# Kernel tuning notes

Measured on AMD Instinct MI355X. Metric: run time of the kernel, lower is better.

The kernel has to match this reference:

```python
import jax, jax.numpy as jnp
import numpy as np

# Static config (matches init_kwargs)
N = 1024        # node_num
F = 64          # input_dim (window length)
D = 64          # dim == embed_dim (heads=1)
TOPK = 20
B = 64
EPS = 1e-5      # BatchNorm eps
NEG_SLOPE = 0.2 # GraphLayer leaky_relu slope


def setup_inputs() -> dict:
    key = jax.random.key(0)
    ks = jax.random.split(key, 12)
    s = lambda fan: 1.0 / np.sqrt(fan)
    inp = {
        'data': jax.random.normal(ks[0], (B, N, F), jnp.float32),
        'org_edge_index': jax.random.randint(ks[1], (2, 2048), 0, N),
        'embedding': jax.random.normal(ks[2], (N, D), jnp.float32) * s(D),   # nn.Embedding(node_num, dim), xavier-ish
        'lin_w': jax.random.normal(ks[3], (F, D), jnp.float32) * s(F),       # GraphLayer lin (bias=False)
        'att_i': jax.random.normal(ks[4], (D,), jnp.float32) * s(D),
        'att_j': jax.random.normal(ks[5], (D,), jnp.float32) * s(D),
        'att_em_i': jax.random.normal(ks[6], (D,), jnp.float32) * s(D),
        'att_em_j': jax.random.normal(ks[7], (D,), jnp.float32) * s(D),
        'gnn_bias': jnp.zeros((D,), jnp.float32),
        'bn1_gamma': jnp.ones((D,), jnp.float32),  # GNNLayer.bn
        'bn1_beta': jnp.zeros((D,), jnp.float32),
        'bn2_gamma': jnp.ones((D,), jnp.float32),  # bn_outlayer_in
        'bn2_beta': jnp.zeros((D,), jnp.float32),
        'out_w': jax.random.normal(ks[8], (D, 1), jnp.float32) * s(D),       # OutLayer Linear(dim, 1)
        'out_b': jnp.zeros((1,), jnp.float32),
    }
    return inp


def _batchnorm(x, gamma, beta, axes):
    # training-mode BatchNorm: batch statistics over `axes`, per-feature affine
    mu = jnp.mean(x, axis=axes, keepdims=True)
    var = jnp.var(x, axis=axes, keepdims=True)
    return gamma * (x - mu) * jax.lax.rsqrt(var + EPS) + beta


def reference(data, org_edge_index, embedding, lin_w, att_i, att_j, att_em_i,
              att_em_j, gnn_bias, bn1_gamma, bn1_beta, bn2_gamma, bn2_beta,
              out_w, out_b):
    # --- dynamic graph construction from embedding cosine similarity ---
    w = jax.lax.stop_gradient(embedding)          # weights_arr.detach()
    nrm = jnp.linalg.norm(w, axis=-1)
    cos = (w @ w.T) / jnp.clip(nrm[:, None] * nrm[None, :], 1e-10)
    _, topi = jax.lax.top_k(cos, TOPK)            # [N, TOPK] neighbors j of each target i
    # (torch code drops edges whose cos value is exactly 0 -- measure-zero with
    #  random embeddings; edge count stays N*TOPK. Self edge i->i is always in topk,
    #  matching remove_self_loops + add_self_loops.)

    # --- GraphLayer (GAT-style, heads=1, concat=False, aggr='add') ---
    xl = jnp.einsum('bnf,fd->bnd', data, lin_w)   # linear transform, [B,N,D]
    xj = xl[:, topi]                               # gather neighbor feats [B,N,TOPK,D]
    ej = embedding[topi]                           # neighbor embeddings [N,TOPK,D]
    # alpha = <key_i, att_i||att_em_i> + <key_j, att_j||att_em_j>
    score = (xl @ att_i)[:, :, None] \
          + (embedding @ att_em_i)[None, :, None] \
          + jnp.einsum('bnkd,d->bnk', xj, att_j) \
          + (ej @ att_em_j)[None]                  # [B,N,TOPK]
    alpha = jax.nn.softmax(jax.nn.leaky_relu(score, NEG_SLOPE), axis=-1)
    gnn = jnp.einsum('bnk,bnkd->bnd', alpha, xj) + gnn_bias

    # GNNLayer.bn: BatchNorm1d over B*N samples, D channels
    gnn = _batchnorm(gnn, bn1_gamma, bn1_beta, axes=(0, 1))

    # --- readout ---
    out = gnn * embedding[None]                    # mul with node embedding
    out = jax.nn.relu(_batchnorm(out, bn2_gamma, bn2_beta, axes=(0, 1)))
    # dropout(0.2) -> identity (eval)
    pred = (out @ out_w + out_b).reshape(B, N)     # OutLayer: Linear(D, 1)
    return pred, out
```

## Files before the change

kernel.cpp:

```cpp
#include <hip/hip_runtime.h>

#define NN 1024
#define KK 20
#define BN 65536
#define NEG_SLOPE 0.2f

typedef unsigned short u16;
typedef unsigned int u32;
typedef unsigned long long u64;
typedef __attribute__((ext_vector_type(8))) short bf8;
typedef __attribute__((ext_vector_type(4))) float f32x4;

__device__ __forceinline__ float bf2f(u16 h) {
    return __uint_as_float(((u32)h) << 16);
}
__device__ __forceinline__ u16 f2bf(float f) {
    u32 u = __float_as_uint(f);
    u32 lsb = (u >> 16) & 1u;
    u += 0x7fffu + lsb;
    return (u16)(u >> 16);
}
__device__ __forceinline__ void up2(u32 w, float& a, float& b) {
    a = __uint_as_float(w << 16);
    b = __uint_as_float(w & 0xffff0000u);
}
__device__ __forceinline__ bool is_bf(const void* g1) {
    return *(const u32*)g1 == 0x3F803F80u;
}
template <bool BF>
__device__ __forceinline__ float ldf(const void* p, size_t i) {
    if (BF) return bf2f(((const u16*)p)[i]);
    return ((const float*)p)[i];
}
template <bool BF>
__device__ __forceinline__ void stf(void* p, size_t i, float v) {
    if (BF) ((u16*)p)[i] = f2bf(v);
    else ((float*)p)[i] = v;
}
template <bool BF>
__device__ __forceinline__ void ldf2(const void* p, size_t pairidx, float& a, float& b) {
    if (BF) {
        u32 w = ((const u32*)p)[pairidx];
        up2(w, a, b);
    } else {
        float2 v = ((const float2*)p)[pairidx];
        a = v.x;
        b = v.y;
    }
}

template <bool BF>
__device__ void k1a_body(const void* emb, const void* aei, const void* aej,
                         u16* nwH, u16* nwL, float* e_i, float* e_j, float* stats) {
    __shared__ float sme[4][64], sm2[4][64];
    int tid = threadIdx.x;
    int lane = tid & 63, wave = tid >> 6;
    int n = blockIdx.x * 4 + wave;
    float v = ldf<BF>(emb, n * 64 + lane);
    sme[wave][lane] = v;
    sm2[wave][lane] = v * v;
    float s2 = v * v;
    float si = v * ldf<BF>(aei, lane);
    float sj = v * ldf<BF>(aej, lane);
#pragma unroll
    for (int off = 32; off; off >>= 1) {
        s2 += __shfl_xor(s2, off, 64);
        si += __shfl_xor(si, off, 64);
        sj += __shfl_xor(sj, off, 64);
    }
    float rq = rsqrtf(fmaxf(s2, 1e-20f));
    float x = v * rq;
    u16 h = f2bf(x);
    nwH[n * 64 + lane] = h;
    nwL[n * 64 + lane] = f2bf(x - bf2f(h));
    if (lane == 0) { e_i[n] = si; e_j[n] = sj; }
    __syncthreads();
    if (tid < 64) {
        float u1 = sme[0][tid] + sme[1][tid] + sme[2][tid] + sme[3][tid];
        atomicAdd(&stats[320 + tid], 64.f * u1);
    } else if (tid < 128) {
        int d = tid - 64;
        float u2 = sm2[0][d] + sm2[1][d] + sm2[2][d] + sm2[3][d];
        atomicAdd(&stats[384 + d], 64.f * u2);
    }
}
__global__ __launch_bounds__(256) void k1a_norm(const void* emb, const void* aei, const void* aej,
                                                const void* probe, u16* nwH, u16* nwL,
                                                float* e_i, float* e_j, float* stats) {
    if (is_bf(probe)) k1a_body<true>(emb, aei, aej, nwH, nwL, e_i, e_j, stats);
    else k1a_body<false>(emb, aei, aej, nwH, nwL, e_i, e_j, stats);
}

__global__ __launch_bounds__(256) void k1b_gram(const u16* __restrict__ nwH,
                                                const u16* __restrict__ nwL,
                                                float* __restrict__ G) {
    int tid = threadIdx.x;
    int lane = tid & 63, wave = tid >> 6;
    int c = lane & 15, quad = lane >> 4;
    int rowblk = blockIdx.x >> 4, colblk = blockIdx.x & 15;
    int arow = rowblk * 64 + wave * 16 + c;
    bf8 aH[2], aL[2];
#pragma unroll
    for (int s = 0; s < 2; ++s) {
        aH[s] = *(const bf8*)(nwH + (size_t)arow * 64 + s * 32 + quad * 8);
        aL[s] = *(const bf8*)(nwL + (size_t)arow * 64 + s * 32 + quad * 8);
    }
    f32x4 acc[4] = {{0.f, 0.f, 0.f, 0.f}, {0.f, 0.f, 0.f, 0.f}, {0.f, 0.f, 0.f, 0.f}, {0.f, 0.f, 0.f, 0.f}};
#pragma unroll
    for (int t = 0; t < 4; ++t) {
        int bnode = colblk * 64 + t * 16 + c;
#pragma unroll
        for (int s = 0; s < 2; ++s) {
            bf8 bH = *(const bf8*)(nwH + (size_t)bnode * 64 + s * 32 + quad * 8);
            bf8 bL = *(const bf8*)(nwL + (size_t)bnode * 64 + s * 32 + quad * 8);
            acc[t] = __builtin_amdgcn_mfma_f32_16x16x32_bf16(aH[s], bH, acc[t], 0, 0, 0);
            acc[t] = __builtin_amdgcn_mfma_f32_16x16x32_bf16(aH[s], bL, acc[t], 0, 0, 0);
            acc[t] = __builtin_amdgcn_mfma_f32_16x16x32_bf16(aL[s], bH, acc[t], 0, 0, 0);
        }
    }
#pragma unroll
    for (int t = 0; t < 4; ++t) {
#pragma unroll
        for (int reg = 0; reg < 4; ++reg) {
            int row = rowblk * 64 + wave * 16 + quad * 4 + reg;
            G[(size_t)row * 1024 + colblk * 64 + t * 16 + c] = acc[t][reg];
        }
    }
}

__device__ void k1c_body(int blk, const float* __restrict__ G, int* __restrict__ topi) {
    int lane = threadIdx.x & 63, wave = threadIdx.x >> 6;
    int n = blk * 4 + wave;
    const f32x4* gp = (const f32x4*)(G + (size_t)n * 1024 + lane * 16);
    f32x4 v0 = gp[0], v1 = gp[1], v2 = gp[2], v3 = gp[3];
    float c[16] = {v0.x, v0.y, v0.z, v0.w, v1.x, v1.y, v1.z, v1.w,
                   v2.x, v2.y, v2.z, v2.w, v3.x, v3.y, v3.z, v3.w};
    u32 o[16];
#pragma unroll
    for (int j = 0; j < 16; ++j) {
        u32 u = __float_as_uint(c[j]);
        o[j] = u ^ (u32)(((int)u >> 31) | 0x80000000);
    }
    unsigned mask = 0u;
    int keep = 0;
    for (int r = 0; r < KK; ++r) {
        u32 bo = 0u;
        int bj = 0;
#pragma unroll
        for (int j = 0; j < 16; ++j) {
            bool t = !((mask >> j) & 1u) && o[j] > bo;
            bo = t ? o[j] : bo;
            bj = t ? j : bj;
        }
        u64 key = ((u64)bo << 32) | (u32)(~(u32)(lane * 16 + bj));
#pragma unroll
        for (int off = 32; off; off >>= 1) {
            u64 ok = __shfl_xor((unsigned long long)key, off, 64);
            key = ok > key ? ok : key;
        }
        int bm = (int)((~(u32)key) & 1023u);
        if ((bm >> 4) == lane) mask |= 1u << (bm & 15);
        if (lane == r) keep = bm;
    }
    if (lane < KK) topi[n * KK + lane] = keep;
}

template <bool BF>
__device__ void k2_body(int blk, const void* data, const void* lin_w, const void* att_i,
                        const void* att_j, u16* xl, float* a_i, float* a_j) {
    __shared__ u16 Bl[64 * 72];
    __shared__ u16 Ct[64 * 72];
    int tid = threadIdx.x;
    {
        int k = tid >> 2, n0 = (tid & 3) * 16;
        if (BF) {
            const u16* lw = (const u16*)lin_w;
#pragma unroll
            for (int i = 0; i < 16; ++i) Bl[(n0 + i) * 72 + k] = lw[k * 64 + n0 + i];
        } else {
            const float* lw = (const float*)lin_w;
#pragma unroll
            for (int i = 0; i < 16; ++i) Bl[(n0 + i) * 72 + k] = f2bf(lw[k * 64 + n0 + i]);
        }
    }
    __syncthreads();
    int lane = tid & 63, wave = tid >> 6;
    int c = lane & 15, quad = lane >> 4;
    int m0 = blk * 64 + wave * 16;
    size_t row = (size_t)(m0 + c);
    f32x4 acc[4] = {{0.f, 0.f, 0.f, 0.f}, {0.f, 0.f, 0.f, 0.f}, {0.f, 0.f, 0.f, 0.f}, {0.f, 0.f, 0.f, 0.f}};
#pragma unroll
    for (int s = 0; s < 2; ++s) {
        bf8 a;
        if (BF) {
            a = *(const bf8*)((const u16*)data + row * 64 + s * 32 + quad * 8);
        } else {
            const float* dp = (const float*)data + row * 64 + s * 32 + quad * 8;
            f32x4 x0 = *(const f32x4*)dp;
            f32x4 x1 = *(const f32x4*)(dp + 4);
            a[0] = (short)f2bf(x0.x); a[1] = (short)f2bf(x0.y);
            a[2] = (short)f2bf(x0.z); a[3] = (short)f2bf(x0.w);
            a[4] = (short)f2bf(x1.x); a[5] = (short)f2bf(x1.y);
            a[6] = (short)f2bf(x1.z); a[7] = (short)f2bf(x1.w);
        }
#pragma unroll
        for (int t = 0; t < 4; ++t) {
            bf8 b = *(const bf8*)&Bl[(t * 16 + c) * 72 + s * 32 + quad * 8];
            acc[t] = __builtin_amdgcn_mfma_f32_16x16x32_bf16(a, b, acc[t], 0, 0, 0);
        }
    }
    float wi[4], wj[4];
#pragma unroll
    for (int t = 0; t < 4; ++t) {
        wi[t] = ldf<BF>(att_i, t * 16 + c);
        wj[t] = ldf<BF>(att_j, t * 16 + c);
    }
    float ai4[4] = {0.f, 0.f, 0.f, 0.f}, aj4[4] = {0.f, 0.f, 0.f, 0.f};
#pragma unroll
    for (int t = 0; t < 4; ++t) {
#pragma unroll
        for (int reg = 0; reg < 4; ++reg) {
            float v = acc[t][reg];
            Ct[(wave * 16 + quad * 4 + reg) * 72 + t * 16 + c] = f2bf(v);
            ai4[reg] += v * wi[t];
            aj4[reg] += v * wj[t];
        }
    }
#pragma unroll
    for (int reg = 0; reg < 4; ++reg) {
#pragma unroll
        for (int off = 1; off < 16; off <<= 1) {
            ai4[reg] += __shfl_xor(ai4[reg], off, 64);
            aj4[reg] += __shfl_xor(aj4[reg], off, 64);
        }
    }
    if (c == 0) {
#pragma unroll
        for (int reg = 0; reg < 4; ++reg) {
            a_i[m0 + quad * 4 + reg] = ai4[reg];
            a_j[m0 + quad * 4 + reg] = aj4[reg];
        }
    }
    __syncthreads();
    {
        int r = tid >> 2, seg = tid & 3;
        uint4 v0 = *(const uint4*)&Ct[r * 72 + seg * 16];
        uint4 v1 = *(const uint4*)&Ct[r * 72 + seg * 16 + 8];
        uint4* dst = (uint4*)xl + ((size_t)(blk * 64 + r) * 8 + seg * 2);
        dst[0] = v0;
        dst[1] = v1;
    }
}

__global__ __launch_bounds__(256) void k12_fused(const void* data, const void* lin_w,
                                                 const void* att_i, const void* att_j,
                                                 const void* probe, u16* xl, float* a_i,
                                                 float* a_j, const float* G, int* topi) {
    if (blockIdx.x < 1024) {
        if (is_bf(probe)) k2_body<true>(blockIdx.x, data, lin_w, att_i, att_j, xl, a_i, a_j);
        else k2_body<false>(blockIdx.x, data, lin_w, att_i, att_j, xl, a_i, a_j);
    } else {
        k1c_body(blockIdx.x - 1024, G, topi);
    }
}

template <bool BF>
__device__ void k3_body(const u16* xl, const int* topi, const float* a_i, const float* a_j,
                        const float* e_i, const float* e_j, const void* emb,
                        const void* gnn_bias, u16* gnnb, float* stats) {
    extern __shared__ char smem[];
    u32* slice = (u32*)smem;
    float* aje = (float*)(smem + 131072);
    float* aie = (float*)(smem + 135168);
    u32* sp = (u32*)(smem + 136192);
    int tid = threadIdx.x;
    int b = blockIdx.x & 63;
    int q = blockIdx.x >> 6;
    int n0 = q * 256;
    const uint4* src = (const uint4*)(xl + ((size_t)b << 16));
    uint4* dst = (uint4*)slice;
#pragma unroll
    for (int r = 0; r < 8; ++r) dst[r * 1024 + tid] = src[r * 1024 + tid];
    aje[tid] = a_j[(b << 10) + tid] + e_j[tid];
    if (tid < 256) aie[tid] = a_i[(b << 10) + n0 + tid] + e_i[n0 + tid];
    __syncthreads();
    int lane = tid & 63, wave = tid >> 6;
    int half = lane >> 5, hl = lane & 31;
    int hwid = wave * 2 + half;
    int nl0 = hwid * 8;
    for (int ii = 0; ii < 8; ++ii) {
        int nl = nl0 + ii;
        int t = (hl < KK) ? topi[(n0 + nl) * KK + hl] : 0;
        float sc = -3e38f;
        if (hl < KK) {
            sc = aie[nl] + aje[t];
            sc = sc >= 0.f ? sc : NEG_SLOPE * sc;
        }
        float m = sc;
#pragma unroll
        for (int off = 16; off; off >>= 1) m = fmaxf(m, __shfl_xor(m, off, 32));
        float p = (hl < KK) ? __expf(sc - m) : 0.f;
        float S = p;
#pragma unroll
        for (int off = 16; off; off >>= 1) S += __shfl_xor(S, off, 32);
        if (hl < KK) sp[(hwid * 8 + ii) * KK + hl] = ((u32)f2bf(p / S) << 16) | (u32)t;
    }
    float bias0, bias1;
    ldf2<BF>(gnn_bias, hl, bias0, bias1);
    float se[10];
#pragma unroll
    for (int s = 0; s < 10; ++s) se[s] = 0.f;
    for (int ii = 0; ii < 8; ++ii) {
        int nl = nl0 + ii;
        int n = n0 + nl;
        int pair = (b << 10) + n;
        const u32* spp = &sp[(hwid * 8 + ii) * KK];
        float a0e = 0.f, a0o = 0.f, a1e = 0.f, a1o = 0.f;
#pragma unroll
        for (int k = 0; k < KK; k += 2) {
            uint2 vv = *(const uint2*)&spp[k];
            u32 w0 = slice[((vv.x & 1023u) << 5) + hl];
            u32 w1 = slice[((vv.y & 1023u) << 5) + hl];
            float p0 = __uint_as_float(vv.x & 0xffff0000u);
            float p1 = __uint_as_float(vv.y & 0xffff0000u);
            a0e += p0 * __uint_as_float(w0 << 16);
            a1e += p0 * __uint_as_float(w0 & 0xffff0000u);
            a0o += p1 * __uint_as_float(w1 << 16);
            a1o += p1 * __uint_as_float(w1 & 0xffff0000u);
        }
        float acc0 = a0e + a0o + bias0;
        float acc1 = a1e + a1o + bias1;
        ((u32*)gnnb)[pair * 32 + hl] = (u32)f2bf(acc0) | ((u32)f2bf(acc1) << 16);
        float em0, em1;
        ldf2<BF>(emb, n * 32 + hl, em0, em1);
        se[0] += acc0; se[1] += acc1;
        se[2] += acc0 * acc0; se[3] += acc1 * acc1;
        float ge0 = acc0 * em0, ge1 = acc1 * em1;
        se[4] += ge0; se[5] += ge1;
        se[6] += ge0 * ge0; se[7] += ge1 * ge1;
        se[8] += ge0 * em0; se[9] += ge1 * em1;
    }
#pragma unroll
    for (int s = 0; s < 10; ++s) se[s] += __shfl_xor(se[s], 32, 64);
    __syncthreads();
    float* ps = (float*)smem;
    if (half == 0) {
#pragma unroll
        for (int s = 0; s < 5; ++s) {
            ps[wave * 320 + s * 64 + 2 * hl] = se[2 * s];
            ps[wave * 320 + s * 64 + 2 * hl + 1] = se[2 * s + 1];
        }
    }
    __syncthreads();
    if (tid < 320) {
        float s = 0.f;
#pragma unroll
        for (int w = 0; w < 16; ++w) s += ps[w * 320 + tid];
        atomicAdd(&stats[tid], s);
    }
}
__global__ __launch_bounds__(1024) void k3_gnn(const u16* xl, const int* topi, const float* a_i,
                                               const float* a_j, const float* e_i, const float* e_j,
                                               const void* emb, const void* gnn_bias, const void* probe,
                                               u16* gnnb, float* stats) {
    if (is_bf(probe)) k3_body<true>(xl, topi, a_i, a_j, e_i, e_j, emb, gnn_bias, gnnb, stats);
    else k3_body<false>(xl, topi, a_i, a_j, e_i, e_j, emb, gnn_bias, gnnb, stats);
}

template <bool BF>
__device__ void k5_body(const void* emb, const float* stats, const void* g1, const void* b1,
                        const void* g2, const void* b2, const void* out_w, const void* out_b,
                        const u16* gnnb, void* dout) {
    int lane = threadIdx.x & 63;
    float P, Q, R;
    {
        int d = lane;
        double inv = 1.0 / 65536.0;
        double S1 = stats[d], S2 = stats[64 + d], T1 = stats[128 + d], T2 = stats[192 + d];
        double T3 = stats[256 + d], U1 = stats[320 + d], U2 = stats[384 + d];
        double mu1 = S1 * inv;
        double var1 = S2 * inv - mu1 * mu1;
        if (var1 < 0.0) var1 = 0.0;
        double r1 = 1.0 / sqrt(var1 + 1e-5);
        double A = (double)ldf<BF>(g1, d) * r1;
        double C = (double)ldf<BF>(b1, d) - A * mu1;
        double E1 = A * T1 + C * U1;
        double mu2 = E1 * inv;
        double E2 = A * A * T2 + 2.0 * A * C * T3 + C * C * U2;
        double var2 = E2 * inv - mu2 * mu2;
        if (var2 < 0.0) var2 = 0.0;
        double r2 = 1.0 / sqrt(var2 + 1e-5);
        double g2r2 = (double)ldf<BF>(g2, d) * r2;
        P = (float)(g2r2 * A);
        Q = (float)(g2r2 * C);
        R = (float)((double)ldf<BF>(b2, d) - g2r2 * mu2);
    }
    int gw = (blockIdx.x * 256 + threadIdx.x) >> 6;
    float wo = ldf<BF>(out_w, lane);
    float ob = ldf<BF>(out_b, 0);
    int row0 = gw * 8;
    for (int i = 0; i < 8; ++i) {
        int row = row0 + i;
        int n = row & 1023;
        float g = bf2f(gnnb[(size_t)row * 64 + lane]);
        float em = ldf<BF>(emb, n * 64 + lane);
        float o = fmaxf(P * g * em + Q * em + R, 0.f);
        stf<BF>(dout, (size_t)BN + (size_t)row * 64 + lane, o);
        float p = o * wo;
#pragma unroll
        for (int off = 32; off; off >>= 1) p += __shfl_xor(p, off, 64);
        if (lane == 0) stf<BF>(dout, row, p + ob);
    }
}
__global__ __launch_bounds__(256) void k5_out(const void* emb, const float* stats, const void* g1,
                                              const void* b1, const void* g2, const void* b2,
                                              const void* out_w, const void* out_b,
                                              const u16* gnnb, void* dout) {
    if (is_bf(g1)) k5_body<true>(emb, stats, g1, b1, g2, b2, out_w, out_b, gnnb, dout);
    else k5_body<false>(emb, stats, g1, b1, g2, b2, out_w, out_b, gnnb, dout);
}

extern "C" void kernel_launch(void* const* d_in, const int* in_sizes, int n_in,
                              void* d_out, int out_size, void* d_ws, size_t ws_size,
                              hipStream_t stream) {
    const void* data = d_in[0];
    const void* emb = d_in[2];
    const void* lin_w = d_in[3];
    const void* att_i = d_in[4];
    const void* att_j = d_in[5];
    const void* att_em_i = d_in[6];
    const void* att_em_j = d_in[7];
    const void* gnn_bias = d_in[8];
    const void* bn1_g = d_in[9];
    const void* bn1_b = d_in[10];
    const void* bn2_g = d_in[11];
    const void* bn2_b = d_in[12];
    const void* out_w = d_in[13];
    const void* out_b = d_in[14];

    char* ws = (char*)d_ws;
    float* a_i = (float*)ws;
    float* a_j = a_i + 65536;
    float* e_i = a_j + 65536;
    float* e_j = e_i + 1024;
    float* stats = e_j + 1024;
    int* topi = (int*)(stats + 448);
    u16* xl = (u16*)(topi + 20480);
    u16* nwH = xl + 4194304;
    u16* nwL = nwH + 65536;
    float* G = (float*)(nwL + 65536);
    u16* gnnb = (u16*)(G + 1048576);

    hipMemsetAsync(stats, 0, 448 * sizeof(float), stream);
    k1a_norm<<<256, 256, 0, stream>>>(emb, att_em_i, att_em_j, bn1_g, nwH, nwL, e_i, e_j, stats);
    k1b_gram<<<256, 256, 0, stream>>>(nwH, nwL, G);
    k12_fused<<<1280, 256, 0, stream>>>(data, lin_w, att_i, att_j, bn1_g, xl, a_i, a_j, G, topi);
    k3_gnn<<<256, 1024, 156672, stream>>>(xl, topi, a_i, a_j, e_i, e_j, emb, gnn_bias, bn1_g,
                                          gnnb, stats);
    k5_out<<<2048, 256, 0, stream>>>(emb, stats, bn1_g, bn1_b, bn2_g, bn2_b, out_w, out_b,
                                     gnnb, d_out);
}
```

Baseline: 160.2 us.

## Drop stats memset, move embedding stats to k3, vectorize k5 output

Replaces the separate memset of the BN statistics buffer with zeroing inside block 0 of the first kernel. The embedding sum and square-sum statistics move from atomics in k1a into the per-block reduction already done in k3, which removes the shared-memory sync there. The readout kernel now handles two channels per lane with paired loads and stores and a 32-lane reduction, and two k3 loops get unroll-by-2 hints. Zeroing stats from block 0 depends on k1a finishing before k3 runs its atomics, which stream ordering guarantees.

```diff
diff --git a/kernel.cpp b/kernel.cpp
--- a/kernel.cpp
+++ b/kernel.cpp
@@ -52,13 +52,13 @@
 template <bool BF>
 __device__ void k1a_body(const void* emb, const void* aei, const void* aej,
                          u16* nwH, u16* nwL, float* e_i, float* e_j, float* stats) {
-    __shared__ float sme[4][64], sm2[4][64];
     int tid = threadIdx.x;
+    if (blockIdx.x == 0) {
+        for (int s = tid; s < 448; s += 256) stats[s] = 0.f;
+    }
     int lane = tid & 63, wave = tid >> 6;
     int n = blockIdx.x * 4 + wave;
     float v = ldf<BF>(emb, n * 64 + lane);
-    sme[wave][lane] = v;
-    sm2[wave][lane] = v * v;
     float s2 = v * v;
     float si = v * ldf<BF>(aei, lane);
     float sj = v * ldf<BF>(aej, lane);
@@ -74,15 +74,6 @@
     nwH[n * 64 + lane] = h;
     nwL[n * 64 + lane] = f2bf(x - bf2f(h));
     if (lane == 0) { e_i[n] = si; e_j[n] = sj; }
-    __syncthreads();
-    if (tid < 64) {
-        float u1 = sme[0][tid] + sme[1][tid] + sme[2][tid] + sme[3][tid];
-        atomicAdd(&stats[320 + tid], 64.f * u1);
-    } else if (tid < 128) {
-        int d = tid - 64;
-        float u2 = sm2[0][d] + sm2[1][d] + sm2[2][d] + sm2[3][d];
-        atomicAdd(&stats[384 + d], 64.f * u2);
-    }
 }
 __global__ __launch_bounds__(256) void k1a_norm(const void* emb, const void* aei, const void* aej,
                                                 const void* probe, u16* nwH, u16* nwL,
@@ -288,6 +279,7 @@
     int half = lane >> 5, hl = lane & 31;
     int hwid = wave * 2 + half;
     int nl0 = hwid * 8;
+#pragma unroll 2
     for (int ii = 0; ii < 8; ++ii) {
         int nl = nl0 + ii;
         int t = (hl < KK) ? topi[(n0 + nl) * KK + hl] : 0;
@@ -307,9 +299,10 @@
     }
     float bias0, bias1;
     ldf2<BF>(gnn_bias, hl, bias0, bias1);
-    float se[10];
-#pragma unroll
-    for (int s = 0; s < 10; ++s) se[s] = 0.f;
+    float se[14];
+#pragma unroll
+    for (int s = 0; s < 14; ++s) se[s] = 0.f;
+#pragma unroll 2
     for (int ii = 0; ii < 8; ++ii) {
         int nl = nl0 + ii;
         int n = n0 + nl;
@@ -339,23 +332,25 @@
         se[4] += ge0; se[5] += ge1;
         se[6] += ge0 * ge0; se[7] += ge1 * ge1;
         se[8] += ge0 * em0; se[9] += ge1 * em1;
-    }
-#pragma unroll
-    for (int s = 0; s < 10; ++s) se[s] += __shfl_xor(se[s], 32, 64);
+        se[10] += em0; se[11] += em1;
+        se[12] += em0 * em0; se[13] += em1 * em1;
+    }
+#pragma unroll
+    for (int s = 0; s < 14; ++s) se[s] += __shfl_xor(se[s], 32, 64);
     __syncthreads();
     float* ps = (float*)smem;
     if (half == 0) {
 #pragma unroll
-        for (int s = 0; s < 5; ++s) {
-            ps[wave * 320 + s * 64 + 2 * hl] = se[2 * s];
-            ps[wave * 320 + s * 64 + 2 * hl + 1] = se[2 * s + 1];
+        for (int s = 0; s < 7; ++s) {
+            ps[wave * 448 + s * 64 + 2 * hl] = se[2 * s];
+            ps[wave * 448 + s * 64 + 2 * hl + 1] = se[2 * s + 1];
         }
     }
     __syncthreads();
-    if (tid < 320) {
+    if (tid < 448) {
         float s = 0.f;
 #pragma unroll
-        for (int w = 0; w < 16; ++w) s += ps[w * 320 + tid];
+        for (int w = 0; w < 16; ++w) s += ps[w * 448 + tid];
         atomicAdd(&stats[tid], s);
     }
 }
@@ -368,48 +363,64 @@
 }
 
 template <bool BF>
+__device__ __forceinline__ void pqr_for(const float* stats, const void* g1, const void* b1,
+                                        const void* g2, const void* b2, int d,
+                                        float& P, float& Q, float& R) {
+    double inv = 1.0 / 65536.0;
+    double S1 = stats[d], S2 = stats[64 + d], T1 = stats[128 + d], T2 = stats[192 + d];
+    double T3 = stats[256 + d], U1 = stats[320 + d], U2 = stats[384 + d];
+    double mu1 = S1 * inv;
+    double var1 = S2 * inv - mu1 * mu1;
+    if (var1 < 0.0) var1 = 0.0;
+    double r1 = 1.0 / sqrt(var1 + 1e-5);
+    double A = (double)ldf<BF>(g1, d) * r1;
+    double C = (double)ldf<BF>(b1, d) - A * mu1;
+    double E1 = A * T1 + C * U1;
+    double mu2 = E1 * inv;
+    double E2 = A * A * T2 + 2.0 * A * C * T3 + C * C * U2;
+    double var2 = E2 * inv - mu2 * mu2;
+    if (var2 < 0.0) var2 = 0.0;
+    double r2 = 1.0 / sqrt(var2 + 1e-5);
+    double g2r2 = (double)ldf<BF>(g2, d) * r2;
+    P = (float)(g2r2 * A);
+    Q = (float)(g2r2 * C);
+    R = (float)((double)ldf<BF>(b2, d) - g2r2 * mu2);
+}
+template <bool BF>
 __device__ void k5_body(const void* emb, const float* stats, const void* g1, const void* b1,
                         const void* g2, const void* b2, const void* out_w, const void* out_b,
                         const u16* gnnb, void* dout) {
-    int lane = threadIdx.x & 63;
-    float P, Q, R;
-    {
-        int d = lane;
-        double inv = 1.0 / 65536.0;
-        double S1 = stats[d], S2 = stats[64 + d], T1 = stats[128 + d], T2 = stats[192 + d];
-        double T3 = stats[256 + d], U1 = stats[320 + d], U2 = stats[384 + d];
-        double mu1 = S1 * inv;
-        double var1 = S2 * inv - mu1 * mu1;
-        if (var1 < 0.0) var1 = 0.0;
-        double r1 = 1.0 / sqrt(var1 + 1e-5);
-        double A = (double)ldf<BF>(g1, d) * r1;
-        double C = (double)ldf<BF>(b1, d) - A * mu1;
-        double E1 = A * T1 + C * U1;
-        double mu2 = E1 * inv;
-        double E2 = A * A * T2 + 2.0 * A * C * T3 + C * C * U2;
-        double var2 = E2 * inv - mu2 * mu2;
-        if (var2 < 0.0) var2 = 0.0;
-        double r2 = 1.0 / sqrt(var2 + 1e-5);
-        double g2r2 = (double)ldf<BF>(g2, d) * r2;
-        P = (float)(g2r2 * A);
-        Q = (float)(g2r2 * C);
-        R = (float)((double)ldf<BF>(b2, d) - g2r2 * mu2);
-    }
-    int gw = (blockIdx.x * 256 + threadIdx.x) >> 6;
-    float wo = ldf<BF>(out_w, lane);
+    int tid = threadIdx.x;
+    int lane = tid & 63;
+    int half = lane >> 5, hl = lane & 31;
+    float P0, Q0, R0, P1, Q1, R1;
+    pqr_for<BF>(stats, g1, b1, g2, b2, 2 * hl, P0, Q0, R0);
+    pqr_for<BF>(stats, g1, b1, g2, b2, 2 * hl + 1, P1, Q1, R1);
+    float wo0, wo1;
+    ldf2<BF>(out_w, hl, wo0, wo1);
     float ob = ldf<BF>(out_b, 0);
+    int gw = (blockIdx.x * 256 + tid) >> 6;
     int row0 = gw * 8;
-    for (int i = 0; i < 8; ++i) {
-        int row = row0 + i;
+    for (int i = 0; i < 4; ++i) {
+        int row = row0 + 2 * i + half;
         int n = row & 1023;
-        float g = bf2f(gnnb[(size_t)row * 64 + lane]);
-        float em = ldf<BF>(emb, n * 64 + lane);
-        float o = fmaxf(P * g * em + Q * em + R, 0.f);
-        stf<BF>(dout, (size_t)BN + (size_t)row * 64 + lane, o);
-        float p = o * wo;
-#pragma unroll
-        for (int off = 32; off; off >>= 1) p += __shfl_xor(p, off, 64);
-        if (lane == 0) stf<BF>(dout, row, p + ob);
+        u32 gv = ((const u32*)gnnb)[row * 32 + hl];
+        float g0, g1v;
+        up2(gv, g0, g1v);
+        float em0, em1;
+        ldf2<BF>(emb, n * 32 + hl, em0, em1);
+        float o0 = fmaxf(P0 * g0 * em0 + Q0 * em0 + R0, 0.f);
+        float o1 = fmaxf(P1 * g1v * em1 + Q1 * em1 + R1, 0.f);
+        if (BF) {
+            ((u32*)dout)[(BN >> 1) + row * 32 + hl] = (u32)f2bf(o0) | ((u32)f2bf(o1) << 16);
+        } else {
+            float2 v2; v2.x = o0; v2.y = o1;
+            ((float2*)dout)[(BN >> 1) + row * 32 + hl] = v2;
+        }
+        float p = o0 * wo0 + o1 * wo1;
+#pragma unroll
+        for (int off = 16; off; off >>= 1) p += __shfl_xor(p, off, 32);
+        if (hl == 0) stf<BF>(dout, row, p + ob);
     }
 }
 __global__ __launch_bounds__(256) void k5_out(const void* emb, const float* stats, const void* g1,
@@ -451,7 +462,6 @@
     float* G = (float*)(nwL + 65536);
     u16* gnnb = (u16*)(G + 1048576);
 
-    hipMemsetAsync(stats, 0, 448 * sizeof(float), stream);
     k1a_norm<<<256, 256, 0, stream>>>(emb, att_em_i, att_em_j, bn1_g, nwH, nwL, e_i, e_j, stats);
     k1b_gram<<<256, 256, 0, stream>>>(nwH, nwL, G);
     k12_fused<<<1280, 256, 0, stream>>>(data, lin_w, att_i, att_j, bn1_g, xl, a_i, a_j, G, topi);
```

After: 153.0 us. -4.5%, faster.
